# Kernel optimization log

Hardware: AMD Instinct MI355X
Metric: run time of the kernel (lower is better)

The kernel has to match this reference:

```python
import jax, jax.numpy as jnp
import numpy as np

CLIP_MIN = 0.0
CLIP_MAX = 1.0
B, T, F, E, CD = 64, 48, 128, 64, 32


def setup_inputs() -> dict:
    key = jax.random.key(0)
    ks = jax.random.split(key, 8)
    return {
        "input_x": jax.random.uniform(ks[0], (B, T, F), dtype=jnp.float32),
        "mask": jax.random.randint(ks[1], (B, T, F), 0, 2, dtype=jnp.int32),
        "embed0": jax.random.normal(ks[2], (F, E), dtype=jnp.float32) * 0.1,
        "embed1": jax.random.normal(ks[3], (F, E), dtype=jnp.float32) * 0.1,
        "embed_missing": jax.random.normal(ks[4], (F, E), dtype=jnp.float32) * 0.1,
        "attention_f_w": jax.random.normal(ks[5], (F, E), dtype=jnp.float32) * 0.1,
        "attention_f_b": jnp.zeros((F,), dtype=jnp.float32),
        "compress_w": jax.random.normal(ks[6], (2 * E, CD), dtype=jnp.float32) * 0.1,
    }


def reference(input_x, mask, embed0, embed1, embed_missing, attention_f_w, attention_f_b, compress_w):
    b, t, f = input_x.shape
    # new_mask: feature observed anywhere in time -> [b, 1, f, 1] (broadcasts over time)
    m = (jnp.sum(mask, axis=-2) != 0).astype(input_x.dtype)[:, None, :, None]
    x = input_x[..., None]  # [b, t, f, 1]
    # interval embedding c: [b, t, f, e]
    c0 = (x - m * CLIP_MIN) * embed0
    c1 = (m * CLIP_MAX - x) * embed1
    c = (c0 + c1) / (CLIP_MAX - CLIP_MIN) + (1.0 - m) * embed_missing
    # pairwise scores: sum_e c_i * c_j * w_i + b_i  (avoids [b,t,f,f,e] materialization)
    scores = jnp.einsum("btie,btje->btij", c * attention_f_w, c) + attention_f_b[:, None]
    scores = jnp.clip(scores, -5.0, 5.0)
    off_diag = 1.0 - jnp.eye(f, dtype=c.dtype)
    masked_exps = jnp.exp(scores) * off_diag
    attn = masked_exps / (jnp.sum(masked_exps, axis=-1, keepdims=True) + 1e-8)  # [b,t,f,f]
    # weighted aggregation: sum_j attn_ij * (c_i * c_j) = c_i * (attn @ c)_i
    agg = c * jnp.einsum("btij,btje->btie", attn, c)
    a = jax.nn.relu(jnp.concatenate([c, agg], axis=-1))  # [b,t,f,2e]
    out = jnp.einsum("btfk,kd->btfd", a, compress_w)
    return out.reshape(b, t, f * compress_w.shape[-1])
```

## Files before the change

### kernel.cpp

```cpp
#include <hip/hip_runtime.h>

#define NB 64
#define NT 48
#define NF 128
#define NE 64
#define NCD 32

#define LOG2E 1.4426950408889634f

typedef __attribute__((ext_vector_type(8))) short bf16x8;
typedef __attribute__((ext_vector_type(4))) float f32x4;
typedef __attribute__((ext_vector_type(2))) uint u32x2;

#define WS_MFLAG 0
#define WS_DB    32768
#define WS_E1B   49152
#define WS_EMB   65536
#define WS_WLB   81920
#define WS_WT    98304
#define WS_BL    106496

__device__ __forceinline__ ushort f2bf(float x) {
    union { float f; uint u; } v; v.f = x;
    uint r = v.u + 0x7fffu + ((v.u >> 16) & 1u);
    return (ushort)(r >> 16);
}
__device__ __forceinline__ uint pk_bf16(float lo, float hi) {
    uint r; asm("v_cvt_pk_bf16_f32 %0, %1, %2" : "=v"(r) : "v"(lo), "v"(hi)); return r;
}
__device__ __forceinline__ float bflo(uint u) { union { uint u; float f; } v; v.u = u << 16; return v.f; }
__device__ __forceinline__ float bfhi(uint u) { union { uint u; float f; } v; v.u = u & 0xffff0000u; return v.f; }

#define TRR(dst, addr, IMM) \
    asm volatile("ds_read_b64_tr_b16 %0, %1 offset:" IMM : "=v"(dst) : "v"(addr))
#define PLSWAP(a, b) asm("v_permlane32_swap_b32 %0, %1" : "+v"(a), "+v"(b))

#define AGG_ISSUE(CR, TB, O0, O1, O2, O3, O4, O5, O6, O7) \
    TRR(CR[0], TB, O0); TRR(CR[1], TB, O1); \
    TRR(CR[2], TB, O2); TRR(CR[3], TB, O3); \
    TRR(CR[4], TB, O4); TRR(CR[5], TB, O5); \
    TRR(CR[6], TB, O6); TRR(CR[7], TB, O7);

#define AGG_CONSUME2(CR, PFA, PFB, AGA, AGB) { \
    union { u32x2 d[2]; bf16x8 v; } q0, q1, q2, q3; \
    q0.d[0] = CR[0]; q0.d[1] = CR[1]; q1.d[0] = CR[2]; q1.d[1] = CR[3]; \
    q2.d[0] = CR[4]; q2.d[1] = CR[5]; q3.d[0] = CR[6]; q3.d[1] = CR[7]; \
    AGA[0] = __builtin_amdgcn_mfma_f32_16x16x32_bf16(q0.v, PFA, AGA[0], 0, 0, 0); \
    AGB[0] = __builtin_amdgcn_mfma_f32_16x16x32_bf16(q0.v, PFB, AGB[0], 0, 0, 0); \
    AGA[1] = __builtin_amdgcn_mfma_f32_16x16x32_bf16(q1.v, PFA, AGA[1], 0, 0, 0); \
    AGB[1] = __builtin_amdgcn_mfma_f32_16x16x32_bf16(q1.v, PFB, AGB[1], 0, 0, 0); \
    AGA[2] = __builtin_amdgcn_mfma_f32_16x16x32_bf16(q2.v, PFA, AGA[2], 0, 0, 0); \
    AGB[2] = __builtin_amdgcn_mfma_f32_16x16x32_bf16(q2.v, PFB, AGB[2], 0, 0, 0); \
    AGA[3] = __builtin_amdgcn_mfma_f32_16x16x32_bf16(q3.v, PFA, AGA[3], 0, 0, 0); \
    AGB[3] = __builtin_amdgcn_mfma_f32_16x16x32_bf16(q3.v, PFB, AGB[3], 0, 0, 0); }

#define PF_BUILD(PF, PP, KS) { \
    uint X0 = PP[4*(KS)], X1 = PP[4*(KS)+1], X2 = PP[4*(KS)+2], X3 = PP[4*(KS)+3]; \
    PLSWAP(X0, X2); PLSWAP(X1, X3); \
    PF.u[0] = X0; PF.u[1] = X1; PF.u[2] = X2; PF.u[3] = X3; }

#define LGKM_WAIT(N) \
    asm volatile("s_waitcnt lgkmcnt(" #N ")" ::: "memory"); \
    __builtin_amdgcn_sched_barrier(0);

__global__ __launch_bounds__(256) void prep_kernel(
    const int* __restrict__ mask, const float* __restrict__ e0, const float* __restrict__ e1,
    const float* __restrict__ em, const float* __restrict__ aw, const float* __restrict__ ab,
    const float* __restrict__ cw,
    uint* __restrict__ mflag, ushort* __restrict__ db, ushort* __restrict__ e1b,
    ushort* __restrict__ emb, ushort* __restrict__ wlb, ushort* __restrict__ wt,
    float* __restrict__ bl)
{
    const int blk = blockIdx.x, tid = threadIdx.x;
    if (blk < 32) {
        int idx = blk * 256 + tid;
        float e1v = e1[idx];
        e1b[idx] = f2bf(e1v);
        emb[idx] = f2bf(em[idx]);
        db[idx]  = f2bf(e0[idx] - e1v);
        wlb[idx] = f2bf(aw[idx] * LOG2E);
    } else if (blk < 64) {
        int idx = (blk - 32) * 256 + tid;
        int b = idx >> 7, f = idx & 127;
        const int* p = mask + b * (NT * NF) + f;
        int s = 0;
#pragma unroll
        for (int t = 0; t < NT; ++t) s += p[t * NF];
        mflag[idx] = (s != 0) ? 1u : 0u;
    } else if (blk < 80) {
        int idx = (blk - 64) * 256 + tid;
        int k = idx >> 5, d = idx & 31;
        int kd;
        if (k < 64) kd = k;
        else {
            int kk = k - 64;
            kd = 64 + ((kk & 51) | ((kk & 4) << 1) | ((kk & 8) >> 1));
        }
        wt[d * 128 + kd] = f2bf(cw[idx]);
    } else {
        if (tid < NF) bl[tid] = ab[tid] * LOG2E;
    }
}

__global__ __launch_bounds__(256, 3) void fused_kernel(
    const float* __restrict__ input_x, const uint* __restrict__ mflag,
    const ushort* __restrict__ db, const ushort* __restrict__ e1b, const ushort* __restrict__ emb,
    const ushort* __restrict__ wlb, const float* __restrict__ blog,
    const ushort* __restrict__ wt, float* __restrict__ out)
{
    __shared__ ushort sC[9248];

    const int tid = threadIdx.x;
    const int bt = blockIdx.x;
    const int b = bt / NT;

    const int wv = tid >> 6, ln = tid & 63;
    const int lr = ln & 15, lg = ln >> 4;
    const int irow0 = wv * 32 + lr;

    const int abase = (lg >> 1) * 2312 + (lr >> 2) * 72 + (lr & 3) * 16 + (lg & 1) * 8;

    const float bl0 = blog[irow0];
    const float bl1 = blog[irow0 + 16];

    bf16x8 cwf[2][2];
#pragma unroll
    for (int g = 0; g < 2; ++g) {
        const int irow = irow0 + g * 16;
        const float x = input_x[bt * NF + irow];
        const ushort* Mrow = (mflag[b * NF + irow] ? e1b : emb) + irow * NE;
        const ushort* Drow = db + irow * NE;
        const ushort* Wrow = wlb + irow * NE;
#pragma unroll
        for (int ks = 0; ks < 2; ++ks) {
            const int eo = ks * 32 + lg * 8;
            uint d4[4], m4[4], w4[4];
            *(uint4*)d4 = *(const uint4*)(Drow + eo);
            *(uint4*)m4 = *(const uint4*)(Mrow + eo);
            *(uint4*)w4 = *(const uint4*)(Wrow + eo);
            uint cb[4]; union { uint u[4]; bf16x8 v; } cu;
#pragma unroll
            for (int j = 0; j < 4; ++j) {
                float clo = fmaf(x, bflo(d4[j]), bflo(m4[j]));
                float chi = fmaf(x, bfhi(d4[j]), bfhi(m4[j]));
                cb[j] = pk_bf16(clo, chi);
                cu.u[j] = pk_bf16(clo * bflo(w4[j]), chi * bfhi(w4[j]));
            }
            cwf[g][ks] = cu.v;
            *(uint4*)&sC[abase + (wv * 2 + g) * 288 + ks * 4624] = *(uint4*)cb;
        }
    }
    __syncthreads();

    uint pp0[16], pp1[16];
    float inv0, inv1;
    {
        f32x4 st[8];
#pragma unroll
        for (int g = 0; g < 2; ++g) {
            const float blv = g ? bl1 : bl0;
            uint* pp = g ? pp1 : pp0;
#pragma unroll
            for (int jt = 0; jt < 8; ++jt) {
                f32x4 a = (f32x4){blv, blv, blv, blv};
                bf16x8 a0 = *(bf16x8*)&sC[abase + jt * 288];
                a = __builtin_amdgcn_mfma_f32_16x16x32_bf16(a0, cwf[g][0], a, 0, 0, 0);
                bf16x8 a1 = *(bf16x8*)&sC[abase + jt * 288 + 4624];
                a = __builtin_amdgcn_mfma_f32_16x16x32_bf16(a1, cwf[g][1], a, 0, 0, 0);
                st[jt] = a;
            }
            const int dt_ = wv * 2 + g;
            float rs0 = 0.f, rs1 = 0.f, rs2 = 0.f, rs3 = 0.f;
#pragma unroll
            for (int jt = 0; jt < 8; ++jt) {
                f32x4 v = st[jt];
                float e0 = exp2f(v[0]);
                float e1 = exp2f(v[1]);
                float e2 = exp2f(v[2]);
                float e3 = exp2f(v[3]);
                if (jt == dt_) {
                    const bool on = (lg == (lr >> 2));
                    e0 = (on && (lr & 3) == 0) ? 0.f : e0;
                    e1 = (on && (lr & 3) == 1) ? 0.f : e1;
                    e2 = (on && (lr & 3) == 2) ? 0.f : e2;
                    e3 = (on && (lr & 3) == 3) ? 0.f : e3;
                }
                rs0 += e0; rs1 += e1; rs2 += e2; rs3 += e3;
                pp[2 * jt]     = pk_bf16(e0, e1);
                pp[2 * jt + 1] = pk_bf16(e2, e3);
            }
            float rs = (rs0 + rs1) + (rs2 + rs3);
            rs += __shfl_xor(rs, 16);
            rs += __shfl_xor(rs, 32);
            if (g) inv1 = 1.0f / (rs + 1e-8f); else inv0 = 1.0f / (rs + 1e-8f);
        }
    }

    f32x4 agA[4], agB[4];
#pragma unroll
    for (int et = 0; et < 4; ++et) { agA[et] = (f32x4){0.f,0.f,0.f,0.f}; agB[et] = (f32x4){0.f,0.f,0.f,0.f}; }
    {
        const uint tb = (uint)(uintptr_t)&sC[0]
                      + 2u * (uint)(72 * (((lg >> 1) << 2) + (lg & 1)) + lr);
        u32x2 cA[8], cB[8];
        union { uint u[4]; bf16x8 v; } pfA0, pfB0, pfA1, pfB1, pfA2, pfB2, pfA3, pfB3;
        PF_BUILD(pfA0, pp0, 0); PF_BUILD(pfB0, pp1, 0);
        AGG_ISSUE(cA, tb, "0", "144", "4624", "4768", "9248", "9392", "13872", "14016");
        PF_BUILD(pfA1, pp0, 1); PF_BUILD(pfB1, pp1, 1);
        AGG_ISSUE(cB, tb, "1152", "1296", "5776", "5920", "10400", "10544", "15024", "15168");
        LGKM_WAIT(8);
        AGG_CONSUME2(cA, pfA0.v, pfB0.v, agA, agB);
        PF_BUILD(pfA2, pp0, 2); PF_BUILD(pfB2, pp1, 2);
        AGG_ISSUE(cA, tb, "2304", "2448", "6928", "7072", "11552", "11696", "16176", "16320");
        LGKM_WAIT(8);
        AGG_CONSUME2(cB, pfA1.v, pfB1.v, agA, agB);
        PF_BUILD(pfA3, pp0, 3); PF_BUILD(pfB3, pp1, 3);
        AGG_ISSUE(cB, tb, "3456", "3600", "8080", "8224", "12704", "12848", "17328", "17472");
        LGKM_WAIT(8);
        AGG_CONSUME2(cA, pfA2.v, pfB2.v, agA, agB);
        LGKM_WAIT(0);
        AGG_CONSUME2(cB, pfA3.v, pfB3.v, agA, agB);
    }

    bf16x8 wf[8];
#pragma unroll
    for (int ks = 0; ks < 4; ++ks)
#pragma unroll
        for (int dt = 0; dt < 2; ++dt)
            wf[ks * 2 + dt] = *(const bf16x8*)(wt + (dt * 16 + lr) * 128 + ks * 32 + lg * 8);

    uint aa0[8], aa1[8];
#pragma unroll
    for (int g = 0; g < 2; ++g) {
        const f32x4* ag = g ? agB : agA;
        const float inv = g ? inv1 : inv0;
        uint* aa = g ? aa1 : aa0;
        const int ebase = (wv * 8 + g * 4 + (lr >> 2)) * 72 + (lr & 3) * 16 + lg * 4;
#pragma unroll
        for (int et = 0; et < 4; ++et) {
            u32x2 cb2 = *(u32x2*)&sC[ebase + et * 2312];
            float a0f = fmaxf(ag[et][0] * inv * bflo(cb2.x), 0.f);
            float a1f = fmaxf(ag[et][1] * inv * bfhi(cb2.x), 0.f);
            float a2f = fmaxf(ag[et][2] * inv * bflo(cb2.y), 0.f);
            float a3f = fmaxf(ag[et][3] * inv * bfhi(cb2.y), 0.f);
            aa[2 * et]     = pk_bf16(a0f, a1f);
            aa[2 * et + 1] = pk_bf16(a2f, a3f);
        }
    }

    float* op = out + bt * (NF * NCD);
#pragma unroll
    for (int g = 0; g < 2; ++g) {
        uint* aa = g ? aa1 : aa0;
        f32x4 oc[2];
        oc[0] = (f32x4){0.f, 0.f, 0.f, 0.f};
        oc[1] = (f32x4){0.f, 0.f, 0.f, 0.f};
#pragma unroll
        for (int ks = 0; ks < 4; ++ks) {
            bf16x8 afr;
            if (ks < 2) {
                const uint4 cc = *(uint4*)&sC[abase + (wv * 2 + g) * 288 + ks * 4624];
                union { uint u[4]; bf16x8 v; } rl;
                asm("v_pk_max_i16 %0, %1, 0" : "=v"(rl.u[0]) : "v"(cc.x));
                asm("v_pk_max_i16 %0, %1, 0" : "=v"(rl.u[1]) : "v"(cc.y));
                asm("v_pk_max_i16 %0, %1, 0" : "=v"(rl.u[2]) : "v"(cc.z));
                asm("v_pk_max_i16 %0, %1, 0" : "=v"(rl.u[3]) : "v"(cc.w));
                afr = rl.v;
            } else {
                const int kk = ks - 2;
                uint Y0 = aa[4 * kk], Y1 = aa[4 * kk + 1], Y2 = aa[4 * kk + 2], Y3 = aa[4 * kk + 3];
                PLSWAP(Y0, Y2);
                PLSWAP(Y1, Y3);
                union { uint u[4]; bf16x8 v; } af;
                af.u[0] = Y0; af.u[1] = Y1; af.u[2] = Y2; af.u[3] = Y3;
                afr = af.v;
            }
            oc[0] = __builtin_amdgcn_mfma_f32_16x16x32_bf16(afr, wf[ks * 2 + 0], oc[0], 0, 0, 0);
            oc[1] = __builtin_amdgcn_mfma_f32_16x16x32_bf16(afr, wf[ks * 2 + 1], oc[1], 0, 0, 0);
        }
#pragma unroll
        for (int dt = 0; dt < 2; ++dt)
#pragma unroll
            for (int r = 0; r < 4; ++r)
                op[(wv * 32 + g * 16 + lg * 4 + r) * NCD + dt * 16 + lr] = oc[dt][r];
    }
}

extern "C" void kernel_launch(void* const* d_in, const int* in_sizes, int n_in,
                              void* d_out, int out_size, void* d_ws, size_t ws_size,
                              hipStream_t stream) {
    const float* input_x       = (const float*)d_in[0];
    const int*   mask          = (const int*)d_in[1];
    const float* embed0        = (const float*)d_in[2];
    const float* embed1        = (const float*)d_in[3];
    const float* embed_missing = (const float*)d_in[4];
    const float* attn_w        = (const float*)d_in[5];
    const float* attn_b        = (const float*)d_in[6];
    const float* compress_w    = (const float*)d_in[7];
    float* out = (float*)d_out;

    char* ws = (char*)d_ws;
    uint*   mflag = (uint*)(ws + WS_MFLAG);
    ushort* dbp   = (ushort*)(ws + WS_DB);
    ushort* e1bp  = (ushort*)(ws + WS_E1B);
    ushort* embp  = (ushort*)(ws + WS_EMB);
    ushort* wlbp  = (ushort*)(ws + WS_WLB);
    ushort* wtp   = (ushort*)(ws + WS_WT);
    float*  blp   = (float*)(ws + WS_BL);

    hipLaunchKernelGGL(prep_kernel, dim3(81), dim3(256), 0, stream,
                       mask, embed0, embed1, embed_missing, attn_w, attn_b, compress_w,
                       mflag, dbp, e1bp, embp, wlbp, wtp, blp);
    hipLaunchKernelGGL(fused_kernel, dim3(NB * NT), dim3(256), 0, stream,
                       input_x, mflag, dbp, e1bp, embp, wlbp, blp, wtp, out);
}
```

Baseline: 44.76 us.

## Process two time steps per 512-thread block and interleave score MFMAs

```diff
diff --git a/kernel.cpp b/kernel.cpp
--- a/kernel.cpp
+++ b/kernel.cpp
@@ -102,21 +102,25 @@
     }
 }
 
-__global__ __launch_bounds__(256, 3) void fused_kernel(
+__global__ __launch_bounds__(512, 4) void fused_kernel(
     const float* __restrict__ input_x, const uint* __restrict__ mflag,
     const ushort* __restrict__ db, const ushort* __restrict__ e1b, const ushort* __restrict__ emb,
     const ushort* __restrict__ wlb, const float* __restrict__ blog,
     const ushort* __restrict__ wt, float* __restrict__ out)
 {
-    __shared__ ushort sC[9248];
+    __shared__ ushort sC[2 * 9248];
 
     const int tid = threadIdx.x;
-    const int bt = blockIdx.x;
-    const int b = bt / NT;
-
-    const int wv = tid >> 6, ln = tid & 63;
+    const int blk = blockIdx.x;
+    const int b   = blk / 24;
+    const int ch  = (tid >> 6) >> 2;
+    const int bt  = b * NT + (blk % 24) * 2 + ch;
+
+    const int wq = (tid >> 6) & 3, ln = tid & 63;
     const int lr = ln & 15, lg = ln >> 4;
-    const int irow0 = wv * 32 + lr;
+    const int irow0 = wq * 32 + lr;
+
+    ushort* sCm = sC + ch * 9248;
 
     const int abase = (lg >> 1) * 2312 + (lr >> 2) * 72 + (lr & 3) * 16 + (lg & 1) * 8;
 
@@ -147,33 +151,40 @@
                 cu.u[j] = pk_bf16(clo * bflo(w4[j]), chi * bfhi(w4[j]));
             }
             cwf[g][ks] = cu.v;
-            *(uint4*)&sC[abase + (wv * 2 + g) * 288 + ks * 4624] = *(uint4*)cb;
+            *(uint4*)&sCm[abase + (wq * 2 + g) * 288 + ks * 4624] = *(uint4*)cb;
         }
     }
     __syncthreads();
 
     uint pp0[16], pp1[16];
-    float inv0, inv1;
-    {
-        f32x4 st[8];
+    float rsa0[4] = {0.f, 0.f, 0.f, 0.f}, rsa1[4] = {0.f, 0.f, 0.f, 0.f};
+#pragma unroll
+    for (int half = 0; half < 2; ++half) {
+        f32x4 stA[4], stB[4];
+#pragma unroll
+        for (int j = 0; j < 4; ++j) {
+            const int jt = half * 4 + j;
+            bf16x8 a0 = *(bf16x8*)&sCm[abase + jt * 288];
+            bf16x8 a1 = *(bf16x8*)&sCm[abase + jt * 288 + 4624];
+            f32x4 a = (f32x4){bl0, bl0, bl0, bl0};
+            a = __builtin_amdgcn_mfma_f32_16x16x32_bf16(a0, cwf[0][0], a, 0, 0, 0);
+            a = __builtin_amdgcn_mfma_f32_16x16x32_bf16(a1, cwf[0][1], a, 0, 0, 0);
+            stA[j] = a;
+            f32x4 c = (f32x4){bl1, bl1, bl1, bl1};
+            c = __builtin_amdgcn_mfma_f32_16x16x32_bf16(a0, cwf[1][0], c, 0, 0, 0);
+            c = __builtin_amdgcn_mfma_f32_16x16x32_bf16(a1, cwf[1][1], c, 0, 0, 0);
+            stB[j] = c;
+        }
 #pragma unroll
         for (int g = 0; g < 2; ++g) {
-            const float blv = g ? bl1 : bl0;
+            f32x4* st = g ? stB : stA;
             uint* pp = g ? pp1 : pp0;
-#pragma unroll
-            for (int jt = 0; jt < 8; ++jt) {
-                f32x4 a = (f32x4){blv, blv, blv, blv};
-                bf16x8 a0 = *(bf16x8*)&sC[abase + jt * 288];
-                a = __builtin_amdgcn_mfma_f32_16x16x32_bf16(a0, cwf[g][0], a, 0, 0, 0);
-                bf16x8 a1 = *(bf16x8*)&sC[abase + jt * 288 + 4624];
-                a = __builtin_amdgcn_mfma_f32_16x16x32_bf16(a1, cwf[g][1], a, 0, 0, 0);
-                st[jt] = a;
-            }
-            const int dt_ = wv * 2 + g;
-            float rs0 = 0.f, rs1 = 0.f, rs2 = 0.f, rs3 = 0.f;
-#pragma unroll
-            for (int jt = 0; jt < 8; ++jt) {
-                f32x4 v = st[jt];
+            float* rsa = g ? rsa1 : rsa0;
+            const int dt_ = wq * 2 + g;
+#pragma unroll
+            for (int j = 0; j < 4; ++j) {
+                const int jt = half * 4 + j;
+                f32x4 v = st[j];
                 float e0 = exp2f(v[0]);
                 float e1 = exp2f(v[1]);
                 float e2 = exp2f(v[2]);
@@ -185,22 +196,26 @@
                     e2 = (on && (lr & 3) == 2) ? 0.f : e2;
                     e3 = (on && (lr & 3) == 3) ? 0.f : e3;
                 }
-                rs0 += e0; rs1 += e1; rs2 += e2; rs3 += e3;
+                rsa[0] += e0; rsa[1] += e1; rsa[2] += e2; rsa[3] += e3;
                 pp[2 * jt]     = pk_bf16(e0, e1);
                 pp[2 * jt + 1] = pk_bf16(e2, e3);
             }
-            float rs = (rs0 + rs1) + (rs2 + rs3);
-            rs += __shfl_xor(rs, 16);
-            rs += __shfl_xor(rs, 32);
-            if (g) inv1 = 1.0f / (rs + 1e-8f); else inv0 = 1.0f / (rs + 1e-8f);
-        }
-    }
+        }
+    }
+    float rs0 = (rsa0[0] + rsa0[1]) + (rsa0[2] + rsa0[3]);
+    rs0 += __shfl_xor(rs0, 16);
+    rs0 += __shfl_xor(rs0, 32);
+    const float inv0 = 1.0f / (rs0 + 1e-8f);
+    float rs1 = (rsa1[0] + rsa1[1]) + (rsa1[2] + rsa1[3]);
+    rs1 += __shfl_xor(rs1, 16);
+    rs1 += __shfl_xor(rs1, 32);
+    const float inv1 = 1.0f / (rs1 + 1e-8f);
 
     f32x4 agA[4], agB[4];
 #pragma unroll
     for (int et = 0; et < 4; ++et) { agA[et] = (f32x4){0.f,0.f,0.f,0.f}; agB[et] = (f32x4){0.f,0.f,0.f,0.f}; }
     {
-        const uint tb = (uint)(uintptr_t)&sC[0]
+        const uint tb = (uint)(uintptr_t)sCm
                       + 2u * (uint)(72 * (((lg >> 1) << 2) + (lg & 1)) + lr);
         u32x2 cA[8], cB[8];
         union { uint u[4]; bf16x8 v; } pfA0, pfB0, pfA1, pfB1, pfA2, pfB2, pfA3, pfB3;
@@ -222,23 +237,16 @@
         AGG_CONSUME2(cB, pfA3.v, pfB3.v, agA, agB);
     }
 
-    bf16x8 wf[8];
-#pragma unroll
-    for (int ks = 0; ks < 4; ++ks)
-#pragma unroll
-        for (int dt = 0; dt < 2; ++dt)
-            wf[ks * 2 + dt] = *(const bf16x8*)(wt + (dt * 16 + lr) * 128 + ks * 32 + lg * 8);
-
     uint aa0[8], aa1[8];
 #pragma unroll
     for (int g = 0; g < 2; ++g) {
         const f32x4* ag = g ? agB : agA;
         const float inv = g ? inv1 : inv0;
         uint* aa = g ? aa1 : aa0;
-        const int ebase = (wv * 8 + g * 4 + (lr >> 2)) * 72 + (lr & 3) * 16 + lg * 4;
+        const int ebase = (wq * 8 + g * 4 + (lr >> 2)) * 72 + (lr & 3) * 16 + lg * 4;
 #pragma unroll
         for (int et = 0; et < 4; ++et) {
-            u32x2 cb2 = *(u32x2*)&sC[ebase + et * 2312];
+            u32x2 cb2 = *(u32x2*)&sCm[ebase + et * 2312];
             float a0f = fmaxf(ag[et][0] * inv * bflo(cb2.x), 0.f);
             float a1f = fmaxf(ag[et][1] * inv * bfhi(cb2.x), 0.f);
             float a2f = fmaxf(ag[et][2] * inv * bflo(cb2.y), 0.f);
@@ -248,42 +256,51 @@
         }
     }
 
+    f32x4 ocA[2], ocB[2];
+    ocA[0] = (f32x4){0.f,0.f,0.f,0.f}; ocA[1] = (f32x4){0.f,0.f,0.f,0.f};
+    ocB[0] = (f32x4){0.f,0.f,0.f,0.f}; ocB[1] = (f32x4){0.f,0.f,0.f,0.f};
+#pragma unroll
+    for (int ks = 0; ks < 4; ++ks) {
+        bf16x8 wf0 = *(const bf16x8*)(wt + lr * 128 + ks * 32 + lg * 8);
+        bf16x8 wf1 = *(const bf16x8*)(wt + (16 + lr) * 128 + ks * 32 + lg * 8);
+        bf16x8 afrA, afrB;
+        if (ks < 2) {
+            const uint4 ccA = *(uint4*)&sCm[abase + (wq * 2 + 0) * 288 + ks * 4624];
+            const uint4 ccB = *(uint4*)&sCm[abase + (wq * 2 + 1) * 288 + ks * 4624];
+            union { uint u[4]; bf16x8 v; } rA, rB;
+            asm("v_pk_max_i16 %0, %1, 0" : "=v"(rA.u[0]) : "v"(ccA.x));
+            asm("v_pk_max_i16 %0, %1, 0" : "=v"(rA.u[1]) : "v"(ccA.y));
+            asm("v_pk_max_i16 %0, %1, 0" : "=v"(rA.u[2]) : "v"(ccA.z));
+            asm("v_pk_max_i16 %0, %1, 0" : "=v"(rA.u[3]) : "v"(ccA.w));
+            asm("v_pk_max_i16 %0, %1, 0" : "=v"(rB.u[0]) : "v"(ccB.x));
+            asm("v_pk_max_i16 %0, %1, 0" : "=v"(rB.u[1]) : "v"(ccB.y));
+            asm("v_pk_max_i16 %0, %1, 0" : "=v"(rB.u[2]) : "v"(ccB.z));
+            asm("v_pk_max_i16 %0, %1, 0" : "=v"(rB.u[3]) : "v"(ccB.w));
+            afrA = rA.v; afrB = rB.v;
+        } else {
+            const int kk = ks - 2;
+            uint YA0 = aa0[4*kk], YA1 = aa0[4*kk+1], YA2 = aa0[4*kk+2], YA3 = aa0[4*kk+3];
+            PLSWAP(YA0, YA2); PLSWAP(YA1, YA3);
+            uint YB0 = aa1[4*kk], YB1 = aa1[4*kk+1], YB2 = aa1[4*kk+2], YB3 = aa1[4*kk+3];
+            PLSWAP(YB0, YB2); PLSWAP(YB1, YB3);
+            union { uint u[4]; bf16x8 v; } fA, fB;
+            fA.u[0] = YA0; fA.u[1] = YA1; fA.u[2] = YA2; fA.u[3] = YA3;
+            fB.u[0] = YB0; fB.u[1] = YB1; fB.u[2] = YB2; fB.u[3] = YB3;
+            afrA = fA.v; afrB = fB.v;
+        }
+        ocA[0] = __builtin_amdgcn_mfma_f32_16x16x32_bf16(afrA, wf0, ocA[0], 0, 0, 0);
+        ocA[1] = __builtin_amdgcn_mfma_f32_16x16x32_bf16(afrA, wf1, ocA[1], 0, 0, 0);
+        ocB[0] = __builtin_amdgcn_mfma_f32_16x16x32_bf16(afrB, wf0, ocB[0], 0, 0, 0);
+        ocB[1] = __builtin_amdgcn_mfma_f32_16x16x32_bf16(afrB, wf1, ocB[1], 0, 0, 0);
+    }
     float* op = out + bt * (NF * NCD);
 #pragma unroll
-    for (int g = 0; g < 2; ++g) {
-        uint* aa = g ? aa1 : aa0;
-        f32x4 oc[2];
-        oc[0] = (f32x4){0.f, 0.f, 0.f, 0.f};
-        oc[1] = (f32x4){0.f, 0.f, 0.f, 0.f};
-#pragma unroll
-        for (int ks = 0; ks < 4; ++ks) {
-            bf16x8 afr;
-            if (ks < 2) {
-                const uint4 cc = *(uint4*)&sC[abase + (wv * 2 + g) * 288 + ks * 4624];
-                union { uint u[4]; bf16x8 v; } rl;
-                asm("v_pk_max_i16 %0, %1, 0" : "=v"(rl.u[0]) : "v"(cc.x));
-                asm("v_pk_max_i16 %0, %1, 0" : "=v"(rl.u[1]) : "v"(cc.y));
-                asm("v_pk_max_i16 %0, %1, 0" : "=v"(rl.u[2]) : "v"(cc.z));
-                asm("v_pk_max_i16 %0, %1, 0" : "=v"(rl.u[3]) : "v"(cc.w));
-                afr = rl.v;
-            } else {
-                const int kk = ks - 2;
-                uint Y0 = aa[4 * kk], Y1 = aa[4 * kk + 1], Y2 = aa[4 * kk + 2], Y3 = aa[4 * kk + 3];
-                PLSWAP(Y0, Y2);
-                PLSWAP(Y1, Y3);
-                union { uint u[4]; bf16x8 v; } af;
-                af.u[0] = Y0; af.u[1] = Y1; af.u[2] = Y2; af.u[3] = Y3;
-                afr = af.v;
-            }
-            oc[0] = __builtin_amdgcn_mfma_f32_16x16x32_bf16(afr, wf[ks * 2 + 0], oc[0], 0, 0, 0);
-            oc[1] = __builtin_amdgcn_mfma_f32_16x16x32_bf16(afr, wf[ks * 2 + 1], oc[1], 0, 0, 0);
-        }
-#pragma unroll
-        for (int dt = 0; dt < 2; ++dt)
-#pragma unroll
-            for (int r = 0; r < 4; ++r)
-                op[(wv * 32 + g * 16 + lg * 4 + r) * NCD + dt * 16 + lr] = oc[dt][r];
-    }
+    for (int dt = 0; dt < 2; ++dt)
+#pragma unroll
+        for (int r = 0; r < 4; ++r) {
+            op[(wq * 32 + lg * 4 + r) * NCD + dt * 16 + lr]      = ocA[dt][r];
+            op[(wq * 32 + 16 + lg * 4 + r) * NCD + dt * 16 + lr] = ocB[dt][r];
+        }
 }
 
 extern "C" void kernel_launch(void* const* d_in, const int* in_sizes, int n_in,
@@ -311,6 +328,6 @@
     hipLaunchKernelGGL(prep_kernel, dim3(81), dim3(256), 0, stream,
                        mask, embed0, embed1, embed_missing, attn_w, attn_b, compress_w,
                        mflag, dbp, e1bp, embp, wlbp, wtp, blp);
-    hipLaunchKernelGGL(fused_kernel, dim3(NB * NT), dim3(256), 0, stream,
+    hipLaunchKernelGGL(fused_kernel, dim3(NB * NT / 2), dim3(512), 0, stream,
                        input_x, mflag, dbp, e1bp, embp, wlbp, blp, wtp, out);
 }
```

Result: slower. 48.69 us (+8.8%).
